# Kernel optimization log

Measured on AMD Instinct MI355X. Metric: run time of the kernel, lower is better.

The kernel has to match this reference:

```python
import jax, jax.numpy as jnp
import numpy as np
import math

B, S, H = 2, 2048, 1024
NH = 16
HD = H // NH  # 64


def setup_inputs() -> dict:
    key = jax.random.key(0)
    ks = jax.random.split(key, 4)
    scale = 1.0 / math.sqrt(H)
    return {
        "hidden_states": jax.random.normal(ks[0], (B, S, H), dtype=jnp.float32),
        "attention_mask": jnp.ones((B, S), dtype=jnp.float32),
        "Wq": jax.random.normal(ks[1], (H, H), dtype=jnp.float32) * scale,
        "bq": jnp.zeros((H,), dtype=jnp.float32),
        "Wk": jax.random.normal(ks[2], (H, H), dtype=jnp.float32) * scale,
        "bk": jnp.zeros((H,), dtype=jnp.float32),
        "Wv": jax.random.normal(ks[3], (H, H), dtype=jnp.float32) * scale,
        "bv": jnp.zeros((H,), dtype=jnp.float32),
    }


def _split_heads(x):
    # [B, S, H] -> [B, NH, S, HD]
    b, s, _ = x.shape
    return x.reshape(b, s, NH, HD).transpose(0, 2, 1, 3)


def reference(hidden_states, attention_mask, Wq, bq, Wk, bk, Wv, bv):
    q = _split_heads(hidden_states @ Wq.T + bq)  # [B, NH, S, HD]
    k = _split_heads(hidden_states @ Wk.T + bk)
    v = _split_heads(hidden_states @ Wv.T + bv)

    # [B, NH, S, S] attention scores
    scores = jnp.einsum("bhqd,bhkd->bhqk", q, k) / math.sqrt(HD)
    # mask: [B, S] -> additive bias [B, 1, 1, S]
    bias = (1.0 - attention_mask)[:, None, None, :] * -10000.0
    probs = jax.nn.softmax(scores + bias, axis=-1)
    # dropout prob = 0.0 (eval semantics) -> identity

    ctx = jnp.einsum("bhqk,bhkd->bhqd", probs, v)  # [B, NH, S, HD]
    ctx = ctx.transpose(0, 2, 1, 3).reshape(hidden_states.shape[0], hidden_states.shape[1], H)
    return ctx
```

## Files before the change

### kernel.cpp

```cpp
#include <hip/hip_runtime.h>
#include <hip/hip_bf16.h>

typedef __bf16 bf16;
typedef __bf16 bf16x4 __attribute__((ext_vector_type(4)));
typedef __bf16 bf16x8 __attribute__((ext_vector_type(8)));
typedef float f32x4 __attribute__((ext_vector_type(4)));

#define GLP(p) ((const __attribute__((address_space(1))) void*)(p))
#define LDSP(p) ((__attribute__((address_space(3))) void*)(p))

__global__ __launch_bounds__(256) void cvt_all_kernel(
    const float* __restrict__ hs, const float* __restrict__ Wq,
    const float* __restrict__ Wk, const float* __restrict__ Wv,
    bf16* __restrict__ Xb, bf16* __restrict__ Wb) {
  int i = blockIdx.x * 256 + threadIdx.x;
  const float* src;
  bf16* dst;
  int off;
  if (i < 1048576) {
    src = hs; dst = Xb; off = i;
  } else {
    int j = i - 1048576;
    int which = j >> 18;
    off = j & 262143;
    src = (which == 0) ? Wq : (which == 1) ? Wk : Wv;
    dst = Wb + (which << 20);
  }
  float4 v = *reinterpret_cast<const float4*>(src + off * 4);
  bf16x4 o = { (bf16)v.x, (bf16)v.y, (bf16)v.z, (bf16)v.w };
  *reinterpret_cast<bf16x4*>(dst + off * 4) = o;
}

__global__ __launch_bounds__(256) void qkv_gemm(
    const bf16* __restrict__ Xb, const bf16* __restrict__ Wb,
    const float* __restrict__ biasq, const float* __restrict__ biask,
    const float* __restrict__ biasv,
    bf16* __restrict__ Qb, bf16* __restrict__ Kb, bf16* __restrict__ Vt) {
  __shared__ __align__(16) bf16 As[128 * 32];
  __shared__ __align__(16) bf16 Bs[128 * 32];
  const int tid = threadIdx.x;
  const int w = tid >> 6, l = tid & 63;
  const int lg = l >> 4, lr = l & 15;
  const int wr = w >> 1, wc = w & 1;
  const int bm = blockIdx.y * 128, bn = blockIdx.x * 128;

  f32x4 acc[4][4] = {};

  #pragma unroll 1
  for (int k0 = 0; k0 < 1024; k0 += 32) {
    #pragma unroll
    for (int i = 0; i < 2; ++i) {
      int row = i * 64 + (tid >> 2);
      int c8 = (tid & 3) * 8;
      __builtin_amdgcn_global_load_lds(GLP(Xb + (bm + row) * 1024 + k0 + c8),
                                       LDSP((char*)As + (i * 256 + w * 64) * 16),
                                       16, 0, 0);
      __builtin_amdgcn_global_load_lds(GLP(Wb + (bn + row) * 1024 + k0 + c8),
                                       LDSP((char*)Bs + (i * 256 + w * 64) * 16),
                                       16, 0, 0);
    }
    __syncthreads();
    bf16x8 af[4], bfq[4];
    #pragma unroll
    for (int t = 0; t < 4; ++t) {
      af[t]  = *reinterpret_cast<const bf16x8*>(
                   reinterpret_cast<const char*>(As) + (wr * 64 + t * 16 + lr) * 64 + lg * 16);
      bfq[t] = *reinterpret_cast<const bf16x8*>(
                   reinterpret_cast<const char*>(Bs) + (wc * 64 + t * 16 + lr) * 64 + lg * 16);
    }
    #pragma unroll
    for (int mt = 0; mt < 4; ++mt)
      #pragma unroll
      for (int nt = 0; nt < 4; ++nt)
        acc[mt][nt] = __builtin_amdgcn_mfma_f32_16x16x32_bf16(af[mt], bfq[nt], acc[mt][nt], 0, 0, 0);
    __syncthreads();
  }

  const int mtx = blockIdx.x >> 3;
  const float* bp = (mtx == 0) ? biasq : (mtx == 1) ? biask : biasv;
  const float scale = (mtx == 0) ? 0.18033688f : 1.0f;
  #pragma unroll
  for (int nt = 0; nt < 4; ++nt) {
    int ng = bn + wc * 64 + nt * 16 + lr;
    int nj = ng & 1023;
    int hh = nj >> 6, d = nj & 63;
    float bias = bp[nj];
    #pragma unroll
    for (int mt = 0; mt < 4; ++mt) {
      int m0 = bm + wr * 64 + mt * 16 + lg * 4;
      int bb = m0 >> 11, s0 = m0 & 2047;
      if (mtx == 2) {
        bf16x4 pk;
        #pragma unroll
        for (int r = 0; r < 4; ++r) pk[r] = (bf16)(acc[mt][nt][r] + bias);
        *reinterpret_cast<bf16x4*>(Vt + (((bb * 16 + hh) * 64 + d) * 2048 + s0)) = pk;
      } else {
        bf16* dst = (mtx == 0) ? Qb : Kb;
        #pragma unroll
        for (int r = 0; r < 4; ++r)
          dst[((bb * 16 + hh) * 2048 + s0 + r) * 64 + d] = (bf16)((acc[mt][nt][r] + bias) * scale);
      }
    }
  }
}

__global__ __launch_bounds__(256) void attn_kernel(
    const bf16* __restrict__ Qb, const bf16* __restrict__ Kb,
    const bf16* __restrict__ Vt, const float* __restrict__ mask,
    float* __restrict__ out) {
  __shared__ __align__(16) bf16 Ks[64 * 64];
  __shared__ __align__(16) bf16 Vs[64 * 64];
  __shared__ __align__(16) bf16 Pl[4][16 * 72];
  const int tid = threadIdx.x;
  const int w = tid >> 6, l = tid & 63;
  const int lg = l >> 4, lr = l & 15;
  const int blk = blockIdx.x;
  const int xcd = blk & 7, i0 = blk >> 3;
  const int bh = xcd * 4 + (i0 >> 5), qt = i0 & 31;
  const int bb = bh >> 4, hh = bh & 15;
  const int q16 = qt * 64 + w * 16;

  const bf16* Qp = Qb + (bh * 2048 + q16) * 64;
  const bf16* Kp = Kb + bh * 2048 * 64;
  const bf16* Vp = Vt + bh * 64 * 2048;
  const float* mp = mask + bb * 2048;

  bool nm = false;
  #pragma unroll
  for (int i = 0; i < 8; ++i) {
    float4 mv = *reinterpret_cast<const float4*>(mp + i * 256 + l * 4);
    nm |= (mv.x != 1.f) | (mv.y != 1.f) | (mv.z != 1.f) | (mv.w != 1.f);
  }
  const bool need_mask = __any(nm);

  bf16x8 aq[2];
  #pragma unroll
  for (int kk = 0; kk < 2; ++kk)
    aq[kk] = *reinterpret_cast<const bf16x8*>(Qp + lr * 64 + kk * 32 + lg * 8);

  f32x4 acc[4] = {};
  float mrun = -3.0e38f;
  float lrun = 0.f;

  const float MB = -10000.0f * 1.44269504f;
  bf16* pw = &Pl[w][0];
  const int srow = tid >> 3, sch = tid & 7;

  #pragma unroll 1
  for (int kv0 = 0; kv0 < 2048; kv0 += 64) {
    #pragma unroll
    for (int p = 0; p < 2; ++p) {
      int rw = p * 32 + srow;
      int chg = sch ^ (rw & 7);
      __builtin_amdgcn_global_load_lds(GLP(Kp + (kv0 + rw) * 64 + chg * 8),
                                       LDSP((char*)Ks + (p * 256 + w * 64) * 16), 16, 0, 0);
      __builtin_amdgcn_global_load_lds(GLP(Vp + rw * 2048 + kv0 + chg * 8),
                                       LDSP((char*)Vs + (p * 256 + w * 64) * 16), 16, 0, 0);
    }
    __syncthreads();

    f32x4 sa[4];
    #pragma unroll
    for (int t = 0; t < 4; ++t) {
      f32x4 z = {};
      #pragma unroll
      for (int kk = 0; kk < 2; ++kk) {
        bf16x8 bk8 = *reinterpret_cast<const bf16x8*>(
            reinterpret_cast<const char*>(Ks) + (t * 16 + lr) * 128 + ((kk * 4 + lg) ^ (lr & 7)) * 16);
        z = __builtin_amdgcn_mfma_f32_16x16x32_bf16(bk8, aq[kk], z, 0, 0, 0);
      }
      sa[t] = z;
    }
    if (need_mask) {
      #pragma unroll
      for (int t = 0; t < 4; ++t) {
        float4 mk = *reinterpret_cast<const float4*>(mp + kv0 + t * 16 + lg * 4);
        sa[t][0] += (1.0f - mk.x) * MB;
        sa[t][1] += (1.0f - mk.y) * MB;
        sa[t][2] += (1.0f - mk.z) * MB;
        sa[t][3] += (1.0f - mk.w) * MB;
      }
    }
    f32x4 mx01 = { fmaxf(sa[0][0], sa[1][0]), fmaxf(sa[0][1], sa[1][1]),
                   fmaxf(sa[0][2], sa[1][2]), fmaxf(sa[0][3], sa[1][3]) };
    f32x4 mx23 = { fmaxf(sa[2][0], sa[3][0]), fmaxf(sa[2][1], sa[3][1]),
                   fmaxf(sa[2][2], sa[3][2]), fmaxf(sa[2][3], sa[3][3]) };
    float rm = fmaxf(fmaxf(fmaxf(mx01[0], mx23[0]), fmaxf(mx01[1], mx23[1])),
                     fmaxf(fmaxf(mx01[2], mx23[2]), fmaxf(mx01[3], mx23[3])));
    rm = fmaxf(rm, __shfl_xor(rm, 16));
    rm = fmaxf(rm, __shfl_xor(rm, 32));
    if (__any(rm > mrun + 8.f)) {
      float mn = fmaxf(mrun, rm);
      float fac = exp2f(mrun - mn);
      mrun = mn;
      lrun *= fac;
      float facq[4];
      #pragma unroll
      for (int r = 0; r < 4; ++r) facq[r] = __shfl(fac, ((l >> 4) << 2) + r);
      #pragma unroll
      for (int nt = 0; nt < 4; ++nt)
        #pragma unroll
        for (int r = 0; r < 4; ++r) acc[nt][r] *= facq[r];
    }
    float rs = 0.f;
    #pragma unroll
    for (int t = 0; t < 4; ++t)
      #pragma unroll
      for (int r = 0; r < 4; ++r) {
        float p = exp2f(sa[t][r] - mrun);
        sa[t][r] = p;
        rs += p;
      }
    rs += __shfl_xor(rs, 16);
    rs += __shfl_xor(rs, 32);
    lrun += rs;
    #pragma unroll
    for (int t = 0; t < 4; ++t) {
      bf16x4 pk = { (bf16)sa[t][0], (bf16)sa[t][1], (bf16)sa[t][2], (bf16)sa[t][3] };
      *reinterpret_cast<bf16x4*>(pw + lr * 72 + t * 16 + lg * 4) = pk;
    }
    asm volatile("" ::: "memory");
    #pragma unroll
    for (int ks = 0; ks < 2; ++ks) {
      bf16x8 pa = *reinterpret_cast<const bf16x8*>(
          reinterpret_cast<const char*>(pw) + lr * 144 + ks * 64 + lg * 16);
      #pragma unroll
      for (int nt = 0; nt < 4; ++nt) {
        bf16x8 bv8 = *reinterpret_cast<const bf16x8*>(
            reinterpret_cast<const char*>(Vs) + (nt * 16 + lr) * 128 + ((ks * 4 + lg) ^ (lr & 7)) * 16);
        acc[nt] = __builtin_amdgcn_mfma_f32_16x16x32_bf16(pa, bv8, acc[nt], 0, 0, 0);
      }
    }
    __syncthreads();
  }

  #pragma unroll
  for (int r = 0; r < 4; ++r) {
    float lq = __shfl(lrun, ((l >> 4) << 2) + r);
    float inv = 1.0f / lq;
    int sq = q16 + lg * 4 + r;
    #pragma unroll
    for (int nt = 0; nt < 4; ++nt) {
      int d = nt * 16 + lr;
      out[((bb * 2048 + sq) * 16 + hh) * 64 + d] = acc[nt][r] * inv;
    }
  }
}

extern "C" void kernel_launch(void* const* d_in, const int* in_sizes, int n_in,
                              void* d_out, int out_size, void* d_ws, size_t ws_size,
                              hipStream_t stream) {
  const float* hs   = (const float*)d_in[0];
  const float* mask = (const float*)d_in[1];
  const float* Wq   = (const float*)d_in[2];
  const float* bq   = (const float*)d_in[3];
  const float* Wk   = (const float*)d_in[4];
  const float* bk   = (const float*)d_in[5];
  const float* Wv   = (const float*)d_in[6];
  const float* bv   = (const float*)d_in[7];
  float* out = (float*)d_out;

  if (ws_size < 39845888u) return;
  bf16* Xb = (bf16*)d_ws;
  bf16* Wb = Xb + 4194304;
  bf16* Qb = Wb + 3145728;
  bf16* Kb = Qb + 4194304;
  bf16* Vt = Kb + 4194304;

  cvt_all_kernel<<<7168, 256, 0, stream>>>(hs, Wq, Wk, Wv, Xb, Wb);
  qkv_gemm<<<dim3(24, 32), 256, 0, stream>>>(Xb, Wb, bq, bk, bv, Qb, Kb, Vt);
  attn_kernel<<<1024, 256, 0, stream>>>(Qb, Kb, Vt, mask, out);
}
```

Measured before the change: 201.4 us.

## Double K-tile depth in QKV GEMM and KV tile in attention with swizzled LDS

The QKV GEMM now stages 64-wide K slices instead of 32 and uses an XOR-swizzled LDS layout to avoid bank conflicts, halving the number of barrier-separated iterations. The attention kernel processes 128 keys per iteration instead of 64, with a wider 16-chunk swizzle on the V tile and a larger per-wave P buffer. This cuts loop and sync overhead and amortizes the softmax rescale check over more keys, at the cost of more LDS and registers, which may lower occupancy.

```diff
diff --git a/kernel.cpp b/kernel.cpp
--- a/kernel.cpp
+++ b/kernel.cpp
@@ -36,8 +36,8 @@
     const float* __restrict__ biasq, const float* __restrict__ biask,
     const float* __restrict__ biasv,
     bf16* __restrict__ Qb, bf16* __restrict__ Kb, bf16* __restrict__ Vt) {
-  __shared__ __align__(16) bf16 As[128 * 32];
-  __shared__ __align__(16) bf16 Bs[128 * 32];
+  __shared__ __align__(16) bf16 As[128 * 64];
+  __shared__ __align__(16) bf16 Bs[128 * 64];
   const int tid = threadIdx.x;
   const int w = tid >> 6, l = tid & 63;
   const int lg = l >> 4, lr = l & 15;
@@ -47,32 +47,37 @@
   f32x4 acc[4][4] = {};
 
   #pragma unroll 1
-  for (int k0 = 0; k0 < 1024; k0 += 32) {
-    #pragma unroll
-    for (int i = 0; i < 2; ++i) {
-      int row = i * 64 + (tid >> 2);
-      int c8 = (tid & 3) * 8;
-      __builtin_amdgcn_global_load_lds(GLP(Xb + (bm + row) * 1024 + k0 + c8),
-                                       LDSP((char*)As + (i * 256 + w * 64) * 16),
-                                       16, 0, 0);
-      __builtin_amdgcn_global_load_lds(GLP(Wb + (bn + row) * 1024 + k0 + c8),
-                                       LDSP((char*)Bs + (i * 256 + w * 64) * 16),
-                                       16, 0, 0);
-    }
-    __syncthreads();
-    bf16x8 af[4], bfq[4];
-    #pragma unroll
-    for (int t = 0; t < 4; ++t) {
-      af[t]  = *reinterpret_cast<const bf16x8*>(
-                   reinterpret_cast<const char*>(As) + (wr * 64 + t * 16 + lr) * 64 + lg * 16);
-      bfq[t] = *reinterpret_cast<const bf16x8*>(
-                   reinterpret_cast<const char*>(Bs) + (wc * 64 + t * 16 + lr) * 64 + lg * 16);
-    }
-    #pragma unroll
-    for (int mt = 0; mt < 4; ++mt)
-      #pragma unroll
-      for (int nt = 0; nt < 4; ++nt)
-        acc[mt][nt] = __builtin_amdgcn_mfma_f32_16x16x32_bf16(af[mt], bfq[nt], acc[mt][nt], 0, 0, 0);
+  for (int k0 = 0; k0 < 1024; k0 += 64) {
+    #pragma unroll
+    for (int p = 0; p < 4; ++p) {
+      int cl = p * 256 + tid;
+      int row = cl >> 3, sch = cl & 7;
+      int cg = (sch ^ (row & 7)) * 8;
+      __builtin_amdgcn_global_load_lds(GLP(Xb + (bm + row) * 1024 + k0 + cg),
+                                       LDSP((char*)As + (p * 256 + w * 64) * 16), 16, 0, 0);
+      __builtin_amdgcn_global_load_lds(GLP(Wb + (bn + row) * 1024 + k0 + cg),
+                                       LDSP((char*)Bs + (p * 256 + w * 64) * 16), 16, 0, 0);
+    }
+    __syncthreads();
+    #pragma unroll
+    for (int kk = 0; kk < 2; ++kk) {
+      bf16x8 af[4], bfq[4];
+      #pragma unroll
+      for (int t = 0; t < 4; ++t) {
+        int arow = wr * 64 + t * 16 + lr;
+        int brow = wc * 64 + t * 16 + lr;
+        int slot = ((kk * 4 + lg) ^ (lr & 7)) * 16;
+        af[t]  = *reinterpret_cast<const bf16x8*>(
+                     reinterpret_cast<const char*>(As) + arow * 128 + slot);
+        bfq[t] = *reinterpret_cast<const bf16x8*>(
+                     reinterpret_cast<const char*>(Bs) + brow * 128 + slot);
+      }
+      #pragma unroll
+      for (int mt = 0; mt < 4; ++mt)
+        #pragma unroll
+        for (int nt = 0; nt < 4; ++nt)
+          acc[mt][nt] = __builtin_amdgcn_mfma_f32_16x16x32_bf16(af[mt], bfq[nt], acc[mt][nt], 0, 0, 0);
+    }
     __syncthreads();
   }
 
@@ -108,9 +113,9 @@
     const bf16* __restrict__ Qb, const bf16* __restrict__ Kb,
     const bf16* __restrict__ Vt, const float* __restrict__ mask,
     float* __restrict__ out) {
-  __shared__ __align__(16) bf16 Ks[64 * 64];
-  __shared__ __align__(16) bf16 Vs[64 * 64];
-  __shared__ __align__(16) bf16 Pl[4][16 * 72];
+  __shared__ __align__(16) bf16 Ks[128 * 64];
+  __shared__ __align__(16) bf16 Vs[64 * 128];
+  __shared__ __align__(16) bf16 Pl[4][16 * 136];
   const int tid = threadIdx.x;
   const int w = tid >> 6, l = tid & 63;
   const int lg = l >> 4, lr = l & 15;
@@ -144,24 +149,26 @@
 
   const float MB = -10000.0f * 1.44269504f;
   bf16* pw = &Pl[w][0];
-  const int srow = tid >> 3, sch = tid & 7;
 
   #pragma unroll 1
-  for (int kv0 = 0; kv0 < 2048; kv0 += 64) {
-    #pragma unroll
-    for (int p = 0; p < 2; ++p) {
-      int rw = p * 32 + srow;
-      int chg = sch ^ (rw & 7);
-      __builtin_amdgcn_global_load_lds(GLP(Kp + (kv0 + rw) * 64 + chg * 8),
-                                       LDSP((char*)Ks + (p * 256 + w * 64) * 16), 16, 0, 0);
-      __builtin_amdgcn_global_load_lds(GLP(Vp + rw * 2048 + kv0 + chg * 8),
-                                       LDSP((char*)Vs + (p * 256 + w * 64) * 16), 16, 0, 0);
-    }
-    __syncthreads();
-
-    f32x4 sa[4];
-    #pragma unroll
-    for (int t = 0; t < 4; ++t) {
+  for (int kv0 = 0; kv0 < 2048; kv0 += 128) {
+    #pragma unroll
+    for (int p = 0; p < 4; ++p) {
+      int cl = p * 256 + tid;
+      int krow = cl >> 3, ksch = cl & 7;
+      __builtin_amdgcn_global_load_lds(
+          GLP(Kp + (kv0 + krow) * 64 + (ksch ^ (krow & 7)) * 8),
+          LDSP((char*)Ks + (p * 256 + w * 64) * 16), 16, 0, 0);
+      int vrow = cl >> 4, vsch = cl & 15;
+      __builtin_amdgcn_global_load_lds(
+          GLP(Vp + vrow * 2048 + kv0 + (vsch ^ (vrow & 15)) * 8),
+          LDSP((char*)Vs + (p * 256 + w * 64) * 16), 16, 0, 0);
+    }
+    __syncthreads();
+
+    f32x4 sa[8];
+    #pragma unroll
+    for (int t = 0; t < 8; ++t) {
       f32x4 z = {};
       #pragma unroll
       for (int kk = 0; kk < 2; ++kk) {
@@ -173,7 +180,7 @@
     }
     if (need_mask) {
       #pragma unroll
-      for (int t = 0; t < 4; ++t) {
+      for (int t = 0; t < 8; ++t) {
         float4 mk = *reinterpret_cast<const float4*>(mp + kv0 + t * 16 + lg * 4);
         sa[t][0] += (1.0f - mk.x) * MB;
         sa[t][1] += (1.0f - mk.y) * MB;
@@ -181,12 +188,13 @@
         sa[t][3] += (1.0f - mk.w) * MB;
       }
     }
-    f32x4 mx01 = { fmaxf(sa[0][0], sa[1][0]), fmaxf(sa[0][1], sa[1][1]),
-                   fmaxf(sa[0][2], sa[1][2]), fmaxf(sa[0][3], sa[1][3]) };
-    f32x4 mx23 = { fmaxf(sa[2][0], sa[3][0]), fmaxf(sa[2][1], sa[3][1]),
-                   fmaxf(sa[2][2], sa[3][2]), fmaxf(sa[2][3], sa[3][3]) };
-    float rm = fmaxf(fmaxf(fmaxf(mx01[0], mx23[0]), fmaxf(mx01[1], mx23[1])),
-                     fmaxf(fmaxf(mx01[2], mx23[2]), fmaxf(mx01[3], mx23[3])));
+    float rm = -3.0e38f;
+    #pragma unroll
+    for (int t = 0; t < 8; t += 2) {
+      f32x4 mx = { fmaxf(sa[t][0], sa[t+1][0]), fmaxf(sa[t][1], sa[t+1][1]),
+                   fmaxf(sa[t][2], sa[t+1][2]), fmaxf(sa[t][3], sa[t+1][3]) };
+      rm = fmaxf(rm, fmaxf(fmaxf(mx[0], mx[1]), fmaxf(mx[2], mx[3])));
+    }
     rm = fmaxf(rm, __shfl_xor(rm, 16));
     rm = fmaxf(rm, __shfl_xor(rm, 32));
     if (__any(rm > mrun + 8.f)) {
@@ -204,7 +212,7 @@
     }
     float rs = 0.f;
     #pragma unroll
-    for (int t = 0; t < 4; ++t)
+    for (int t = 0; t < 8; ++t)
       #pragma unroll
       for (int r = 0; r < 4; ++r) {
         float p = exp2f(sa[t][r] - mrun);
@@ -215,19 +223,19 @@
     rs += __shfl_xor(rs, 32);
     lrun += rs;
     #pragma unroll
-    for (int t = 0; t < 4; ++t) {
+    for (int t = 0; t < 8; ++t) {
       bf16x4 pk = { (bf16)sa[t][0], (bf16)sa[t][1], (bf16)sa[t][2], (bf16)sa[t][3] };
-      *reinterpret_cast<bf16x4*>(pw + lr * 72 + t * 16 + lg * 4) = pk;
+      *reinterpret_cast<bf16x4*>(pw + lr * 136 + t * 16 + lg * 4) = pk;
     }
     asm volatile("" ::: "memory");
     #pragma unroll
-    for (int ks = 0; ks < 2; ++ks) {
+    for (int ks = 0; ks < 4; ++ks) {
       bf16x8 pa = *reinterpret_cast<const bf16x8*>(
-          reinterpret_cast<const char*>(pw) + lr * 144 + ks * 64 + lg * 16);
+          reinterpret_cast<const char*>(pw) + lr * 272 + ks * 64 + lg * 16);
       #pragma unroll
       for (int nt = 0; nt < 4; ++nt) {
         bf16x8 bv8 = *reinterpret_cast<const bf16x8*>(
-            reinterpret_cast<const char*>(Vs) + (nt * 16 + lr) * 128 + ((ks * 4 + lg) ^ (lr & 7)) * 16);
+            reinterpret_cast<const char*>(Vs) + (nt * 16 + lr) * 256 + ((ks * 4 + lg) ^ lr) * 16);
         acc[nt] = __builtin_amdgcn_mfma_f32_16x16x32_bf16(pa, bv8, acc[nt], 0, 0, 0);
       }
     }
```

Result: slower. 210.6 us (+4.6%).
